# Performance work log

Hardware: AMD Instinct MI355X
Metric: run time of the kernel (lower is better)

## Reference

```python
import jax, jax.numpy as jnp
import numpy as np

# dims: B batches, N points/batch, S sampled points/batch, M image-projected points/batch,
# V voxels, (H,Wd) range-image size, HID hidden size, NSC scales, NCLS classes
B, N, S, M, V, H, Wd, HID, NSC, NCLS = 2, 120000, 40000, 30000, 100000, 256, 1024, 128, 4, 20


def setup_inputs() -> dict:
    key = jax.random.key(0)
    ks = jax.random.split(key, 24)
    f = jnp.float32
    w = lambda k, shp: (0.02 * jax.random.normal(k, shp, f))
    rows = jax.random.randint(ks[10], (B, M), 0, H, jnp.int32)
    cols = jax.random.randint(ks[11], (B, M), 0, Wd, jnp.int32)
    return {
        "pts_feat_layers": jax.random.normal(ks[0], (NSC, V, HID), f),
        "pts_sample_feat": jax.random.normal(ks[1], (NSC, B * S, HID), f),
        "img_latent_full": jax.random.normal(ks[2], (B, HID, H, Wd), f),
        "img_feat_layers": jax.random.normal(ks[3], (NSC, B * M, HID), f),
        "leaner_W": w(ks[4], (NSC, HID, HID)), "leaner_b": jnp.zeros((NSC, HID), f),
        "fcs1_W": w(ks[5], (NSC, 2 * HID, HID)), "fcs1_b": jnp.zeros((NSC, HID), f),
        "fcs2_W": w(ks[6], (NSC, HID, HID)), "fcs2_b": jnp.zeros((NSC, HID), f),
        "cls_W1": w(ks[7], (NSC * HID, 128)), "cls_b1": jnp.zeros((128,), f),
        "cls_W2": w(ks[8], (128, NCLS)), "cls_b2": jnp.zeros((NCLS,), f),
        "points_img": jnp.stack([rows, cols], axis=-1),              # [B,M,2]
        "point2img_index": jax.random.randint(ks[12], (B, M), 0, N, jnp.int32),
        "sample_index": jax.random.randint(ks[13], (B, S), 0, N, jnp.int32),
        "coors_inv": jax.random.randint(ks[14], (B * N,), 0, V, jnp.int32),
    }


def reference(pts_feat_layers, pts_sample_feat, img_latent_full, img_feat_layers,
              leaner_W, leaner_b, fcs1_W, fcs1_b, fcs2_W, fcs2_b,
              cls_W1, cls_b1, cls_W2, cls_b2,
              points_img, point2img_index, sample_index, coors_inv):
    dt = img_latent_full.dtype
    img_hw = jnp.transpose(img_latent_full, (0, 2, 3, 1))  # [B,H,Wd,HID]
    bar = jnp.arange(B)[:, None]
    # gather image features at projected pixel coords: [B,M,HID]
    img_at_pts = img_hw[bar, points_img[:, :, 0], points_img[:, :, 1]]
    # scatter image features to per-point slots (pts_img_batch_new): [B,N,HID]
    pimg = jax.vmap(lambda idx, v: jnp.zeros((N, HID), dt).at[idx].set(v))(point2img_index, img_at_pts)

    fuse_feats, enc_feats = [], []
    for i in range(NSC):
        # p2img_mapping_spsample: output values depend only on sampled feats + image gather
        sf = pts_sample_feat[i].reshape(B, S, HID)
        sp = jax.vmap(lambda idx, v: jnp.zeros((N, HID), dt).at[idx].set(v))(sample_index, sf)
        sp = sp + pimg  # sample_point_feat == sample_point_feat_f  [B,N,HID]
        # scatter fused point features back into voxel features, then gather per point
        pts_feat = pts_feat_layers[i].at[coors_inv].set(sp.reshape(B * N, HID))
        pts_point = pts_feat[coors_inv].reshape(B, N, HID)
        # p2img_mapping: gather the image-projected points per batch  [B*M,HID]
        pts_g = jnp.take_along_axis(pts_point, point2img_index[:, :, None], axis=1).reshape(B * M, HID)
        fl = jax.nn.relu(pts_g @ leaner_W[i] + leaner_b[i])
        fc = jnp.concatenate([img_feat_layers[i], fl], axis=1) @ fcs1_W[i] + fcs1_b[i]
        fw = jax.nn.sigmoid(fc @ fcs2_W[i] + fcs2_b[i])
        fuse_feats.append(jax.nn.relu(fc * fw))
        enc_feats.append(sp.reshape(B * N, HID))

    seg = jnp.concatenate(fuse_feats, axis=1)                       # [B*M, NSC*HID]
    img_seg_logits = jax.nn.relu(seg @ cls_W1 + cls_b1) @ cls_W2 + cls_b2  # [B*M, NCLS]
    output_3d = jnp.concatenate(enc_feats, axis=1)                  # [B*N, NSC*HID]
    return img_seg_logits, output_3d
```

## Files before the change

### kernel.cpp

```cpp
#include <hip/hip_runtime.h>
#include <hip/hip_bf16.h>
#include <math.h>

#define B_    2
#define N_    120000
#define S_    40000
#define M_    30000
#define V_    100000
#define H_    256
#define WD_   1024
#define HID_  128
#define NSC_  4
#define NCLS_ 20
#define BM_   60000
#define BS_   80000
#define BN_   240000

typedef __attribute__((ext_vector_type(8))) short bfrag8;
typedef __attribute__((ext_vector_type(4))) float facc4;
typedef __attribute__((ext_vector_type(4))) unsigned short usvec4;

__device__ __forceinline__ unsigned short f2bf(float f){
  unsigned u = __builtin_bit_cast(unsigned, f);
  u += 0x7fffu + ((u >> 16) & 1u);
  return (unsigned short)(u >> 16);
}
__device__ __forceinline__ float bf2f(unsigned short s){
  return __builtin_bit_cast(float, ((unsigned)s) << 16);
}

__global__ __launch_bounds__(256) void k_front(
    const float* __restrict__ img, const int* __restrict__ ptsimg,
    unsigned short* __restrict__ iap,
    const int* __restrict__ p2i, const int* __restrict__ si,
    const int* __restrict__ ci,
    int* __restrict__ win_p, int* __restrict__ win_s, int* __restrict__ win_c,
    const float* __restrict__ lW, const float* __restrict__ f1W,
    const float* __restrict__ f2W, const float* __restrict__ c1W,
    const float* __restrict__ c2W,
    unsigned short* __restrict__ lwT, unsigned short* __restrict__ f1T,
    unsigned short* __restrict__ f2T, unsigned short* __restrict__ c1T,
    unsigned short* __restrict__ c2T){
  int bid = blockIdx.x;
  if (bid < 938){
    int t = bid * 256 + threadIdx.x;
    if (t < BM_) atomicMax(&win_p[(t / M_) * N_ + p2i[t]], t);
    if (t < BS_) atomicMax(&win_s[(t / S_) * N_ + si[t]], t);
    if (t < BN_) atomicMax(&win_c[ci[t]], t);
    return;
  }
  if (bid < 2228){
    int t = (bid - 938) * 256 + threadIdx.x;
    if (t < 65536){
      int i = t >> 14, r = t & 16383, n = r >> 7, k = r & 127;
      lwT[i * 16384 + n * 128 + k] = f2bf(lW[i * 16384 + k * 128 + n]);
    } else if (t < 196608){
      int e = t - 65536;
      int i = e >> 15, r = e & 32767, n = r >> 8, k = r & 255;
      f1T[i * 32768 + n * 256 + k] = f2bf(f1W[i * 32768 + k * 128 + n]);
    } else if (t < 262144){
      int e = t - 196608;
      int i = e >> 14, r = e & 16383, n = r >> 7, k = r & 127;
      f2T[i * 16384 + n * 128 + k] = f2bf(f2W[i * 16384 + k * 128 + n]);
    } else if (t < 327680){
      int e = t - 262144;
      int n = e >> 9, k = e & 511;
      c1T[n * 512 + k] = f2bf(c1W[k * 128 + n]);
    } else if (t < 330240){
      int e = t - 327680;
      int n = e >> 7, k = e & 127;
      c2T[n * 128 + k] = f2bf(c2W[k * NCLS_ + n]);
    }
    return;
  }
  {
    int t = (bid - 2228) * 256 + threadIdx.x;
    int row = t >> 5, h4 = (t & 31) * 4;
    int b = row / M_;
    int r = ptsimg[row * 2 + 0];
    int c = ptsimg[row * 2 + 1];
    const float* base = img + (((size_t)b * HID_ + h4) * H_ + r) * WD_ + c;
    const size_t st = (size_t)H_ * WD_;
    float v0 = base[0], v1 = base[st], v2 = base[2 * st], v3 = base[3 * st];
    usvec4 o = {f2bf(v0), f2bf(v1), f2bf(v2), f2bf(v3)};
    *(usvec4*)(iap + (size_t)row * HID_ + h4) = o;
    return;
  }
}

__global__ __launch_bounds__(256) void k_o3d(const float* __restrict__ samp,
    const int* __restrict__ win_s, const int* __restrict__ win_p,
    const unsigned short* __restrict__ iap, float* __restrict__ o3d){
  int t = blockIdx.x * 256 + threadIdx.x;
  int j = t >> 5, q = t & 31;
  int sj = win_s[j], pj = win_p[j];
  facc4 iv = {0.f, 0.f, 0.f, 0.f};
  if (pj >= 0){
    usvec4 u = *(const usvec4*)(iap + (size_t)pj * HID_ + q * 4);
    iv.x = bf2f(u.x); iv.y = bf2f(u.y); iv.z = bf2f(u.z); iv.w = bf2f(u.w);
  }
  #pragma unroll
  for (int i = 0; i < NSC_; i++){
    facc4 v = iv;
    if (sj >= 0){
      facc4 s = *(const facc4*)(samp + ((size_t)i * BS_ + sj) * HID_ + q * 4);
      v += s;
    }
    __builtin_nontemporal_store(v, (facc4*)(o3d + (size_t)j * (NSC_ * HID_) + i * HID_ + q * 4));
  }
}

__global__ __launch_bounds__(256, 3) void k_scales(
    const float* __restrict__ samp, const unsigned short* __restrict__ iap,
    const int* __restrict__ win_p, const int* __restrict__ win_s,
    const int* __restrict__ win_c, const int* __restrict__ p2i,
    const int* __restrict__ ci, const float* __restrict__ imgf,
    const unsigned short* __restrict__ lwT, const float* __restrict__ lb,
    const unsigned short* __restrict__ f1T, const float* __restrict__ f1b,
    const unsigned short* __restrict__ f2T, const float* __restrict__ f2b,
    unsigned short* __restrict__ seg){
  __shared__ char lds[49152];
  char* actL = lds + 32768;
  const int i  = blockIdx.x & 3;
  const int rb = blockIdx.x >> 2;
  const int lane = threadIdx.x & 63, wv = threadIdx.x >> 6;
  const int rl = lane & 15, kg = lane >> 4;
  const int rowBase = rb * 64 + wv * 16;
  const int row = rowBase + rl;
  const bool rv = row < BM_;
  const int lr = wv * 16 + rl;

  {
    const char* src = (const char*)(lwT + (size_t)i * 16384);
    for (int c = threadIdx.x; c < 2048; c += 256){
      int byte = c << 4; int n = byte >> 8;
      *(bfrag8*)(lds + (byte ^ ((n & 7) << 4))) = *(const bfrag8*)(src + byte);
    }
  }
  bfrag8 afr[4];
  {
    int g = 0;
    if (rv){ int b = row >= M_; g = win_c[ci[b * N_ + p2i[row]]]; }
    int sj = rv ? win_s[g] : -1;
    int pj = rv ? win_p[g] : -1;
    const float* sp = samp + ((size_t)i * BS_ + (sj < 0 ? 0 : sj)) * HID_;
    const unsigned short* pp = iap + (size_t)(pj < 0 ? 0 : pj) * HID_;
    #pragma unroll
    for (int kc = 0; kc < 4; kc++){
      int k0 = kc * 32 + kg * 8;
      facc4 s0 = {0,0,0,0}, s1 = {0,0,0,0};
      if (sj >= 0){ s0 = *(const facc4*)(sp + k0); s1 = *(const facc4*)(sp + k0 + 4); }
      float g0=0,g1=0,g2=0,g3=0,g4=0,g5=0,g6=0,g7=0;
      if (pj >= 0){
        usvec4 u0 = *(const usvec4*)(pp + k0);
        usvec4 u1 = *(const usvec4*)(pp + k0 + 4);
        g0=bf2f(u0.x); g1=bf2f(u0.y); g2=bf2f(u0.z); g3=bf2f(u0.w);
        g4=bf2f(u1.x); g5=bf2f(u1.y); g6=bf2f(u1.z); g7=bf2f(u1.w);
      }
      bfrag8 a;
      a[0]=(short)f2bf(s0.x+g0); a[1]=(short)f2bf(s0.y+g1);
      a[2]=(short)f2bf(s0.z+g2); a[3]=(short)f2bf(s0.w+g3);
      a[4]=(short)f2bf(s1.x+g4); a[5]=(short)f2bf(s1.y+g5);
      a[6]=(short)f2bf(s1.z+g6); a[7]=(short)f2bf(s1.w+g7);
      afr[kc] = a;
    }
  }
  __syncthreads();
  facc4 accL[8];
  #pragma unroll
  for (int ct = 0; ct < 8; ct++) accL[ct] = (facc4){0.f,0.f,0.f,0.f};
  #pragma unroll
  for (int kc = 0; kc < 4; kc++){
    int k0 = kc * 32 + kg * 8;
    #pragma unroll
    for (int ct = 0; ct < 8; ct++){
      int col = ct * 16 + rl;
      int byte = (col << 8) + (k0 << 1);
      bfrag8 b = *(const bfrag8*)(lds + (byte ^ ((col & 7) << 4)));
      accL[ct] = __builtin_amdgcn_mfma_f32_16x16x32_bf16(afr[kc], b, accL[ct], 0, 0, 0);
    }
  }
  __syncthreads();
  {
    const float* bias = lb + i * HID_;
    #pragma unroll
    for (int ct = 0; ct < 8; ct++){
      int col = ct * 16 + rl;
      float bv = bias[col];
      #pragma unroll
      for (int r = 0; r < 4; r++){
        int ar = wv * 16 + kg * 4 + r;
        float v = accL[ct][r] + bv; v = v > 0.f ? v : 0.f;
        int byte = ar * 256 + col * 2;
        *(unsigned short*)(actL + (byte ^ ((ar & 7) << 4))) = f2bf(v);
      }
    }
    const char* src = (const char*)(f1T + (size_t)i * 32768);
    for (int c = threadIdx.x; c < 2048; c += 256){
      int n = c >> 4, off = (c & 15) << 4;
      *(bfrag8*)(lds + ((n * 256 + off) ^ ((n & 7) << 4))) =
          *(const bfrag8*)(src + (size_t)n * 512 + off);
    }
  }
  __syncthreads();
  facc4 accF[8];
  #pragma unroll
  for (int ct = 0; ct < 8; ct++) accF[ct] = (facc4){0.f,0.f,0.f,0.f};
  {
    const float* a1 = imgf + ((size_t)i * BM_ + (rv ? row : 0)) * HID_;
    #pragma unroll
    for (int kc = 0; kc < 4; kc++){
      int kk = kc * 32 + kg * 8;
      bfrag8 a = (bfrag8){0,0,0,0,0,0,0,0};
      if (rv){
        facc4 s0 = *(const facc4*)(a1 + kk);
        facc4 s1 = *(const facc4*)(a1 + kk + 4);
        a[0]=(short)f2bf(s0.x); a[1]=(short)f2bf(s0.y); a[2]=(short)f2bf(s0.z); a[3]=(short)f2bf(s0.w);
        a[4]=(short)f2bf(s1.x); a[5]=(short)f2bf(s1.y); a[6]=(short)f2bf(s1.z); a[7]=(short)f2bf(s1.w);
      }
      #pragma unroll
      for (int ct = 0; ct < 8; ct++){
        int col = ct * 16 + rl;
        int byte = (col << 8) + (kk << 1);
        bfrag8 b = *(const bfrag8*)(lds + (byte ^ ((col & 7) << 4)));
        accF[ct] = __builtin_amdgcn_mfma_f32_16x16x32_bf16(a, b, accF[ct], 0, 0, 0);
      }
    }
  }
  __syncthreads();
  {
    const char* src = (const char*)(f1T + (size_t)i * 32768) + 256;
    for (int c = threadIdx.x; c < 2048; c += 256){
      int n = c >> 4, off = (c & 15) << 4;
      *(bfrag8*)(lds + ((n * 256 + off) ^ ((n & 7) << 4))) =
          *(const bfrag8*)(src + (size_t)n * 512 + off);
    }
  }
  __syncthreads();
  #pragma unroll
  for (int kc = 0; kc < 4; kc++){
    int kl = kc * 32 + kg * 8;
    int byteA = lr * 256 + kl * 2;
    bfrag8 a = *(const bfrag8*)(actL + (byteA ^ ((lr & 7) << 4)));
    #pragma unroll
    for (int ct = 0; ct < 8; ct++){
      int col = ct * 16 + rl;
      int byte = (col << 8) + (kl << 1);
      bfrag8 b = *(const bfrag8*)(lds + (byte ^ ((col & 7) << 4)));
      accF[ct] = __builtin_amdgcn_mfma_f32_16x16x32_bf16(a, b, accF[ct], 0, 0, 0);
    }
  }
  __syncthreads();
  {
    const float* bias = f1b + i * HID_;
    #pragma unroll
    for (int ct = 0; ct < 8; ct++){
      int col = ct * 16 + rl;
      float bv = bias[col];
      #pragma unroll
      for (int r = 0; r < 4; r++){
        int ar = wv * 16 + kg * 4 + r;
        float v = accF[ct][r] + bv;
        accF[ct][r] = v;
        int byte = ar * 256 + col * 2;
        *(unsigned short*)(actL + (byte ^ ((ar & 7) << 4))) = f2bf(v);
      }
    }
    const char* src = (const char*)(f2T + (size_t)i * 16384);
    for (int c = threadIdx.x; c < 2048; c += 256){
      int byte = c << 4; int n = byte >> 8;
      *(bfrag8*)(lds + (byte ^ ((n & 7) << 4))) = *(const bfrag8*)(src + byte);
    }
  }
  __syncthreads();
  facc4 accT[8];
  #pragma unroll
  for (int ct = 0; ct < 8; ct++) accT[ct] = (facc4){0.f,0.f,0.f,0.f};
  #pragma unroll
  for (int kc = 0; kc < 4; kc++){
    int kk = kc * 32 + kg * 8;
    int byteA = lr * 256 + kk * 2;
    bfrag8 a = *(const bfrag8*)(actL + (byteA ^ ((lr & 7) << 4)));
    #pragma unroll
    for (int ct = 0; ct < 8; ct++){
      int col = ct * 16 + rl;
      int byte = (col << 8) + (kk << 1);
      bfrag8 b = *(const bfrag8*)(lds + (byte ^ ((col & 7) << 4)));
      accT[ct] = __builtin_amdgcn_mfma_f32_16x16x32_bf16(a, b, accT[ct], 0, 0, 0);
    }
  }
  {
    const float* bias2 = f2b + i * HID_;
    #pragma unroll
    for (int ct = 0; ct < 8; ct++){
      int col = ct * 16 + rl;
      float bv2 = bias2[col];
      #pragma unroll
      for (int r = 0; r < 4; r++){
        int orow = rowBase + kg * 4 + r;
        if (orow < BM_){
          float tv = accT[ct][r] + bv2;
          float fw = 1.f / (1.f + expf(-tv));
          float u = accF[ct][r] * fw;
          u = u > 0.f ? u : 0.f;
          seg[(size_t)orow * (NSC_ * HID_) + i * HID_ + col] = f2bf(u);
        }
      }
    }
  }
}

__global__ __launch_bounds__(256, 3) void k_cls(const unsigned short* __restrict__ seg,
    const unsigned short* __restrict__ c1T, const float* __restrict__ c1b,
    const unsigned short* __restrict__ c2T, const float* __restrict__ c2b,
    float* __restrict__ logits){
  __shared__ char lds[49152];
  char* actL = lds + 32768;
  const int lane = threadIdx.x & 63, wv = threadIdx.x >> 6;
  const int rl = lane & 15, kg = lane >> 4;
  const int rowBase = blockIdx.x * 64 + wv * 16;
  const int row = rowBase + rl;
  const bool rv = row < BM_;
  const unsigned short* ar = seg + (size_t)(rv ? row : 0) * 512;
  facc4 acc[8];
  #pragma unroll
  for (int ct = 0; ct < 8; ct++) acc[ct] = (facc4){0.f,0.f,0.f,0.f};
  for (int ph = 0; ph < 4; ph++){
    if (ph) __syncthreads();
    for (int c = threadIdx.x; c < 2048; c += 256){
      int n = c >> 4, off = (c & 15) << 4;
      *(bfrag8*)(lds + ((n * 256 + off) ^ ((n & 7) << 4))) =
          *(const bfrag8*)((const char*)c1T + (size_t)n * 1024 + ph * 256 + off);
    }
    __syncthreads();
    #pragma unroll
    for (int kc = 0; kc < 4; kc++){
      int kl = kc * 32 + kg * 8;
      bfrag8 a = (bfrag8){0,0,0,0,0,0,0,0};
      if (rv) a = *(const bfrag8*)(ar + ph * 128 + kl);
      #pragma unroll
      for (int ct = 0; ct < 8; ct++){
        int col = ct * 16 + rl;
        int byte = (col << 8) + (kl << 1);
        bfrag8 b = *(const bfrag8*)(lds + (byte ^ ((col & 7) << 4)));
        acc[ct] = __builtin_amdgcn_mfma_f32_16x16x32_bf16(a, b, acc[ct], 0, 0, 0);
      }
    }
  }
  __syncthreads();
  #pragma unroll
  for (int ct = 0; ct < 8; ct++){
    int col = ct * 16 + rl;
    float bv = c1b[col];
    #pragma unroll
    for (int r = 0; r < 4; r++){
      int arr = wv * 16 + kg * 4 + r;
      float v = acc[ct][r] + bv; v = v > 0.f ? v : 0.f;
      int byte = arr * 256 + col * 2;
      *(unsigned short*)(actL + (byte ^ ((arr & 7) << 4))) = f2bf(v);
    }
  }
  for (int c = threadIdx.x; c < 320; c += 256)
    *(bfrag8*)(lds + (c << 4)) = *(const bfrag8*)((const char*)c2T + (c << 4));
  __syncthreads();
  {
    int t = threadIdx.x;
    int lrd = t >> 2, n0 = (t & 3) * 5;
    int orow = blockIdx.x * 64 + lrd;
    if (orow < BM_){
      float accD[5];
      #pragma unroll
      for (int q = 0; q < 5; q++) accD[q] = c2b[n0 + q];
      #pragma unroll
      for (int k8 = 0; k8 < 16; k8++){
        int byteA = lrd * 256 + (k8 << 4);
        bfrag8 hv = *(const bfrag8*)(actL + (byteA ^ ((lrd & 7) << 4)));
        #pragma unroll
        for (int q = 0; q < 5; q++){
          bfrag8 w8 = *(const bfrag8*)(lds + (n0 + q) * 256 + (k8 << 4));
          #pragma unroll
          for (int e = 0; e < 8; e++)
            accD[q] += bf2f((unsigned short)hv[e]) * bf2f((unsigned short)w8[e]);
        }
      }
      #pragma unroll
      for (int q = 0; q < 5; q++)
        logits[(size_t)orow * NCLS_ + n0 + q] = accD[q];
    }
  }
}

extern "C" void kernel_launch(void* const* d_in, const int* in_sizes, int n_in,
                              void* d_out, int out_size, void* d_ws, size_t ws_size,
                              hipStream_t stream){
  const float* samp = (const float*)d_in[1];
  const float* img  = (const float*)d_in[2];
  const float* imgf = (const float*)d_in[3];
  const float* lW   = (const float*)d_in[4];
  const float* lb   = (const float*)d_in[5];
  const float* f1W  = (const float*)d_in[6];
  const float* f1b  = (const float*)d_in[7];
  const float* f2W  = (const float*)d_in[8];
  const float* f2b  = (const float*)d_in[9];
  const float* c1W  = (const float*)d_in[10];
  const float* c1b  = (const float*)d_in[11];
  const float* c2W  = (const float*)d_in[12];
  const float* c2b  = (const float*)d_in[13];
  const int* ptsimg = (const int*)d_in[14];
  const int* p2i    = (const int*)d_in[15];
  const int* si     = (const int*)d_in[16];
  const int* ci     = (const int*)d_in[17];

  char* ws = (char*)d_ws;
  int*   win_p = (int*)(ws + 0);
  int*   win_s = (int*)(ws + 960000);
  int*   win_c = (int*)(ws + 1920000);
  unsigned short* iap = (unsigned short*)(ws + 2320128);
  unsigned short* seg = (unsigned short*)(ws + 17680384);
  unsigned short* lwT = (unsigned short*)(ws + 79120512);
  unsigned short* f1T = lwT + 65536;
  unsigned short* f2T = f1T + 131072;
  unsigned short* c1T = f2T + 65536;
  unsigned short* c2T = c1T + 65536;

  float* logits = (float*)d_out;
  float* o3d    = (float*)d_out + (size_t)BM_ * NCLS_;

  (void)hipMemsetAsync(ws, 0xFF, 2320000, stream);
  k_front  <<<9728,  256, 0, stream>>>(img, ptsimg, iap, p2i, si, ci,
                                       win_p, win_s, win_c,
                                       lW, f1W, f2W, c1W, c2W,
                                       lwT, f1T, f2T, c1T, c2T);
  k_o3d    <<<30000, 256, 0, stream>>>(samp, win_s, win_p, iap, o3d);
  k_scales <<<3752,  256, 0, stream>>>(samp, iap, win_p, win_s, win_c, p2i, ci,
                                       imgf, lwT, lb, f1T, f1b, f2T, f2b, seg);
  k_cls    <<<938,   256, 0, stream>>>(seg, c1T, c1b, c2T, c2b, logits);
}
```

Baseline: 459.9 us.

## Fuse per-scale MLP and classifier into one kernel, batch o3d rows

Merges k_scales and k_cls into a single kernel. Each 64-row block loops over the four scales and accumulates the first classifier layer in registers, so the bf16 seg intermediate is no longer written to and re-read from global memory. Weights are staged into LDS in 64-column halves, which cuts LDS to 32KB and allows occupancy hint 5, at the cost of extra barriers and a serialized scale loop with fewer blocks. k_o3d now handles four output rows per thread, and the image gather in k_front handles both batches per thread, which reduces launch and index overhead.

```diff
diff --git a/kernel.cpp b/kernel.cpp
--- a/kernel.cpp
+++ b/kernel.cpp
@@ -27,6 +27,30 @@
 }
 __device__ __forceinline__ float bf2f(unsigned short s){
   return __builtin_bit_cast(float, ((unsigned)s) << 16);
+}
+
+__device__ __forceinline__ void stageW(char* wbuf, const char* src, int nstride, int tid){
+  #pragma unroll
+  for (int c0 = 0; c0 < 4; c0++){
+    int c = c0 * 256 + tid;
+    int nloc = c >> 4, off = (c & 15) << 4;
+    *(bfrag8*)(wbuf + (((nloc << 8) + off) ^ ((nloc & 7) << 4))) =
+        *(const bfrag8*)(src + (size_t)nloc * nstride + off);
+  }
+}
+
+__device__ __forceinline__ void mfmaHalf(facc4* acc4, const bfrag8* afr,
+                                         const char* wbuf, int rl, int kg){
+  #pragma unroll
+  for (int kc = 0; kc < 4; kc++){
+    int k2 = (kc * 32 + kg * 8) << 1;
+    #pragma unroll
+    for (int ctl = 0; ctl < 4; ctl++){
+      int nloc = ctl * 16 + rl;
+      bfrag8 b = *(const bfrag8*)(wbuf + (((nloc << 8) + k2) ^ ((nloc & 7) << 4)));
+      acc4[ctl] = __builtin_amdgcn_mfma_f32_16x16x32_bf16(afr[kc], b, acc4[ctl], 0, 0, 0);
+    }
+  }
 }
 
 __global__ __launch_bounds__(256) void k_front(
@@ -75,15 +99,18 @@
   }
   {
     int t = (bid - 2228) * 256 + threadIdx.x;
-    int row = t >> 5, h4 = (t & 31) * 4;
-    int b = row / M_;
-    int r = ptsimg[row * 2 + 0];
-    int c = ptsimg[row * 2 + 1];
-    const float* base = img + (((size_t)b * HID_ + h4) * H_ + r) * WD_ + c;
+    int r0 = t >> 5, h4 = (t & 31) * 4;
     const size_t st = (size_t)H_ * WD_;
-    float v0 = base[0], v1 = base[st], v2 = base[2 * st], v3 = base[3 * st];
-    usvec4 o = {f2bf(v0), f2bf(v1), f2bf(v2), f2bf(v3)};
-    *(usvec4*)(iap + (size_t)row * HID_ + h4) = o;
+    #pragma unroll
+    for (int half = 0; half < 2; half++){
+      int row = r0 + half * 30000;
+      int r = ptsimg[row * 2 + 0];
+      int c = ptsimg[row * 2 + 1];
+      const float* base = img + (((size_t)half * HID_ + h4) * H_ + r) * WD_ + c;
+      float v0 = base[0], v1 = base[st], v2 = base[2 * st], v3 = base[3 * st];
+      usvec4 o = {f2bf(v0), f2bf(v1), f2bf(v2), f2bf(v3)};
+      *(usvec4*)(iap + (size_t)row * HID_ + h4) = o;
+    }
     return;
   }
 }
@@ -92,25 +119,35 @@
     const int* __restrict__ win_s, const int* __restrict__ win_p,
     const unsigned short* __restrict__ iap, float* __restrict__ o3d){
   int t = blockIdx.x * 256 + threadIdx.x;
-  int j = t >> 5, q = t & 31;
-  int sj = win_s[j], pj = win_p[j];
-  facc4 iv = {0.f, 0.f, 0.f, 0.f};
-  if (pj >= 0){
-    usvec4 u = *(const usvec4*)(iap + (size_t)pj * HID_ + q * 4);
-    iv.x = bf2f(u.x); iv.y = bf2f(u.y); iv.z = bf2f(u.z); iv.w = bf2f(u.w);
+  int jg = t >> 5, q = t & 31;
+  int j0 = jg << 2;
+  int sjv[4], pjv[4];
+  #pragma unroll
+  for (int jj = 0; jj < 4; jj++){ sjv[jj] = win_s[j0 + jj]; pjv[jj] = win_p[j0 + jj]; }
+  facc4 iv[4];
+  #pragma unroll
+  for (int jj = 0; jj < 4; jj++){
+    facc4 v = {0.f, 0.f, 0.f, 0.f};
+    if (pjv[jj] >= 0){
+      usvec4 u = *(const usvec4*)(iap + (size_t)pjv[jj] * HID_ + q * 4);
+      v.x = bf2f(u.x); v.y = bf2f(u.y); v.z = bf2f(u.z); v.w = bf2f(u.w);
+    }
+    iv[jj] = v;
   }
   #pragma unroll
   for (int i = 0; i < NSC_; i++){
-    facc4 v = iv;
-    if (sj >= 0){
-      facc4 s = *(const facc4*)(samp + ((size_t)i * BS_ + sj) * HID_ + q * 4);
-      v += s;
-    }
-    __builtin_nontemporal_store(v, (facc4*)(o3d + (size_t)j * (NSC_ * HID_) + i * HID_ + q * 4));
-  }
-}
-
-__global__ __launch_bounds__(256, 3) void k_scales(
+    #pragma unroll
+    for (int jj = 0; jj < 4; jj++){
+      facc4 v = iv[jj];
+      if (sjv[jj] >= 0)
+        v += *(const facc4*)(samp + ((size_t)i * BS_ + sjv[jj]) * HID_ + q * 4);
+      __builtin_nontemporal_store(v,
+          (facc4*)(o3d + (size_t)(j0 + jj) * (NSC_ * HID_) + i * HID_ + q * 4));
+    }
+  }
+}
+
+__global__ __launch_bounds__(256, 5) void k_fused(
     const float* __restrict__ samp, const unsigned short* __restrict__ iap,
     const int* __restrict__ win_p, const int* __restrict__ win_s,
     const int* __restrict__ win_c, const int* __restrict__ p2i,
@@ -118,254 +155,210 @@
     const unsigned short* __restrict__ lwT, const float* __restrict__ lb,
     const unsigned short* __restrict__ f1T, const float* __restrict__ f1b,
     const unsigned short* __restrict__ f2T, const float* __restrict__ f2b,
-    unsigned short* __restrict__ seg){
-  __shared__ char lds[49152];
-  char* actL = lds + 32768;
-  const int i  = blockIdx.x & 3;
-  const int rb = blockIdx.x >> 2;
-  const int lane = threadIdx.x & 63, wv = threadIdx.x >> 6;
-  const int rl = lane & 15, kg = lane >> 4;
-  const int rowBase = rb * 64 + wv * 16;
-  const int row = rowBase + rl;
-  const bool rv = row < BM_;
-  const int lr = wv * 16 + rl;
-
-  {
-    const char* src = (const char*)(lwT + (size_t)i * 16384);
-    for (int c = threadIdx.x; c < 2048; c += 256){
-      int byte = c << 4; int n = byte >> 8;
-      *(bfrag8*)(lds + (byte ^ ((n & 7) << 4))) = *(const bfrag8*)(src + byte);
-    }
-  }
-  bfrag8 afr[4];
-  {
-    int g = 0;
-    if (rv){ int b = row >= M_; g = win_c[ci[b * N_ + p2i[row]]]; }
-    int sj = rv ? win_s[g] : -1;
-    int pj = rv ? win_p[g] : -1;
-    const float* sp = samp + ((size_t)i * BS_ + (sj < 0 ? 0 : sj)) * HID_;
-    const unsigned short* pp = iap + (size_t)(pj < 0 ? 0 : pj) * HID_;
-    #pragma unroll
-    for (int kc = 0; kc < 4; kc++){
-      int k0 = kc * 32 + kg * 8;
-      facc4 s0 = {0,0,0,0}, s1 = {0,0,0,0};
-      if (sj >= 0){ s0 = *(const facc4*)(sp + k0); s1 = *(const facc4*)(sp + k0 + 4); }
-      float g0=0,g1=0,g2=0,g3=0,g4=0,g5=0,g6=0,g7=0;
-      if (pj >= 0){
-        usvec4 u0 = *(const usvec4*)(pp + k0);
-        usvec4 u1 = *(const usvec4*)(pp + k0 + 4);
-        g0=bf2f(u0.x); g1=bf2f(u0.y); g2=bf2f(u0.z); g3=bf2f(u0.w);
-        g4=bf2f(u1.x); g5=bf2f(u1.y); g6=bf2f(u1.z); g7=bf2f(u1.w);
-      }
-      bfrag8 a;
-      a[0]=(short)f2bf(s0.x+g0); a[1]=(short)f2bf(s0.y+g1);
-      a[2]=(short)f2bf(s0.z+g2); a[3]=(short)f2bf(s0.w+g3);
-      a[4]=(short)f2bf(s1.x+g4); a[5]=(short)f2bf(s1.y+g5);
-      a[6]=(short)f2bf(s1.z+g6); a[7]=(short)f2bf(s1.w+g7);
-      afr[kc] = a;
-    }
-  }
-  __syncthreads();
-  facc4 accL[8];
-  #pragma unroll
-  for (int ct = 0; ct < 8; ct++) accL[ct] = (facc4){0.f,0.f,0.f,0.f};
-  #pragma unroll
-  for (int kc = 0; kc < 4; kc++){
-    int k0 = kc * 32 + kg * 8;
-    #pragma unroll
-    for (int ct = 0; ct < 8; ct++){
-      int col = ct * 16 + rl;
-      int byte = (col << 8) + (k0 << 1);
-      bfrag8 b = *(const bfrag8*)(lds + (byte ^ ((col & 7) << 4)));
-      accL[ct] = __builtin_amdgcn_mfma_f32_16x16x32_bf16(afr[kc], b, accL[ct], 0, 0, 0);
-    }
-  }
-  __syncthreads();
-  {
-    const float* bias = lb + i * HID_;
-    #pragma unroll
-    for (int ct = 0; ct < 8; ct++){
-      int col = ct * 16 + rl;
-      float bv = bias[col];
-      #pragma unroll
-      for (int r = 0; r < 4; r++){
-        int ar = wv * 16 + kg * 4 + r;
-        float v = accL[ct][r] + bv; v = v > 0.f ? v : 0.f;
-        int byte = ar * 256 + col * 2;
-        *(unsigned short*)(actL + (byte ^ ((ar & 7) << 4))) = f2bf(v);
-      }
-    }
-    const char* src = (const char*)(f1T + (size_t)i * 32768);
-    for (int c = threadIdx.x; c < 2048; c += 256){
-      int n = c >> 4, off = (c & 15) << 4;
-      *(bfrag8*)(lds + ((n * 256 + off) ^ ((n & 7) << 4))) =
-          *(const bfrag8*)(src + (size_t)n * 512 + off);
-    }
-  }
-  __syncthreads();
-  facc4 accF[8];
-  #pragma unroll
-  for (int ct = 0; ct < 8; ct++) accF[ct] = (facc4){0.f,0.f,0.f,0.f};
-  {
-    const float* a1 = imgf + ((size_t)i * BM_ + (rv ? row : 0)) * HID_;
-    #pragma unroll
-    for (int kc = 0; kc < 4; kc++){
-      int kk = kc * 32 + kg * 8;
-      bfrag8 a = (bfrag8){0,0,0,0,0,0,0,0};
-      if (rv){
-        facc4 s0 = *(const facc4*)(a1 + kk);
-        facc4 s1 = *(const facc4*)(a1 + kk + 4);
-        a[0]=(short)f2bf(s0.x); a[1]=(short)f2bf(s0.y); a[2]=(short)f2bf(s0.z); a[3]=(short)f2bf(s0.w);
-        a[4]=(short)f2bf(s1.x); a[5]=(short)f2bf(s1.y); a[6]=(short)f2bf(s1.z); a[7]=(short)f2bf(s1.w);
-      }
-      #pragma unroll
-      for (int ct = 0; ct < 8; ct++){
-        int col = ct * 16 + rl;
-        int byte = (col << 8) + (kk << 1);
-        bfrag8 b = *(const bfrag8*)(lds + (byte ^ ((col & 7) << 4)));
-        accF[ct] = __builtin_amdgcn_mfma_f32_16x16x32_bf16(a, b, accF[ct], 0, 0, 0);
-      }
-    }
-  }
-  __syncthreads();
-  {
-    const char* src = (const char*)(f1T + (size_t)i * 32768) + 256;
-    for (int c = threadIdx.x; c < 2048; c += 256){
-      int n = c >> 4, off = (c & 15) << 4;
-      *(bfrag8*)(lds + ((n * 256 + off) ^ ((n & 7) << 4))) =
-          *(const bfrag8*)(src + (size_t)n * 512 + off);
-    }
-  }
-  __syncthreads();
-  #pragma unroll
-  for (int kc = 0; kc < 4; kc++){
-    int kl = kc * 32 + kg * 8;
-    int byteA = lr * 256 + kl * 2;
-    bfrag8 a = *(const bfrag8*)(actL + (byteA ^ ((lr & 7) << 4)));
-    #pragma unroll
-    for (int ct = 0; ct < 8; ct++){
-      int col = ct * 16 + rl;
-      int byte = (col << 8) + (kl << 1);
-      bfrag8 b = *(const bfrag8*)(lds + (byte ^ ((col & 7) << 4)));
-      accF[ct] = __builtin_amdgcn_mfma_f32_16x16x32_bf16(a, b, accF[ct], 0, 0, 0);
-    }
-  }
-  __syncthreads();
-  {
-    const float* bias = f1b + i * HID_;
-    #pragma unroll
-    for (int ct = 0; ct < 8; ct++){
-      int col = ct * 16 + rl;
-      float bv = bias[col];
-      #pragma unroll
-      for (int r = 0; r < 4; r++){
-        int ar = wv * 16 + kg * 4 + r;
-        float v = accF[ct][r] + bv;
-        accF[ct][r] = v;
-        int byte = ar * 256 + col * 2;
-        *(unsigned short*)(actL + (byte ^ ((ar & 7) << 4))) = f2bf(v);
-      }
-    }
-    const char* src = (const char*)(f2T + (size_t)i * 16384);
-    for (int c = threadIdx.x; c < 2048; c += 256){
-      int byte = c << 4; int n = byte >> 8;
-      *(bfrag8*)(lds + (byte ^ ((n & 7) << 4))) = *(const bfrag8*)(src + byte);
-    }
-  }
-  __syncthreads();
-  facc4 accT[8];
-  #pragma unroll
-  for (int ct = 0; ct < 8; ct++) accT[ct] = (facc4){0.f,0.f,0.f,0.f};
-  #pragma unroll
-  for (int kc = 0; kc < 4; kc++){
-    int kk = kc * 32 + kg * 8;
-    int byteA = lr * 256 + kk * 2;
-    bfrag8 a = *(const bfrag8*)(actL + (byteA ^ ((lr & 7) << 4)));
-    #pragma unroll
-    for (int ct = 0; ct < 8; ct++){
-      int col = ct * 16 + rl;
-      int byte = (col << 8) + (kk << 1);
-      bfrag8 b = *(const bfrag8*)(lds + (byte ^ ((col & 7) << 4)));
-      accT[ct] = __builtin_amdgcn_mfma_f32_16x16x32_bf16(a, b, accT[ct], 0, 0, 0);
-    }
-  }
-  {
-    const float* bias2 = f2b + i * HID_;
-    #pragma unroll
-    for (int ct = 0; ct < 8; ct++){
-      int col = ct * 16 + rl;
-      float bv2 = bias2[col];
-      #pragma unroll
-      for (int r = 0; r < 4; r++){
-        int orow = rowBase + kg * 4 + r;
-        if (orow < BM_){
-          float tv = accT[ct][r] + bv2;
-          float fw = 1.f / (1.f + expf(-tv));
-          float u = accF[ct][r] * fw;
-          u = u > 0.f ? u : 0.f;
-          seg[(size_t)orow * (NSC_ * HID_) + i * HID_ + col] = f2bf(u);
-        }
-      }
-    }
-  }
-}
-
-__global__ __launch_bounds__(256, 3) void k_cls(const unsigned short* __restrict__ seg,
     const unsigned short* __restrict__ c1T, const float* __restrict__ c1b,
     const unsigned short* __restrict__ c2T, const float* __restrict__ c2b,
     float* __restrict__ logits){
-  __shared__ char lds[49152];
-  char* actL = lds + 32768;
-  const int lane = threadIdx.x & 63, wv = threadIdx.x >> 6;
+  __shared__ char lds[32768];
+  char* wbuf = lds;
+  char* actL = lds + 16384;
+  const int tid = threadIdx.x;
+  const int lane = tid & 63, wv = tid >> 6;
   const int rl = lane & 15, kg = lane >> 4;
   const int rowBase = blockIdx.x * 64 + wv * 16;
   const int row = rowBase + rl;
   const bool rv = row < BM_;
-  const unsigned short* ar = seg + (size_t)(rv ? row : 0) * 512;
-  facc4 acc[8];
-  #pragma unroll
-  for (int ct = 0; ct < 8; ct++) acc[ct] = (facc4){0.f,0.f,0.f,0.f};
-  for (int ph = 0; ph < 4; ph++){
-    if (ph) __syncthreads();
-    for (int c = threadIdx.x; c < 2048; c += 256){
-      int n = c >> 4, off = (c & 15) << 4;
-      *(bfrag8*)(lds + ((n * 256 + off) ^ ((n & 7) << 4))) =
-          *(const bfrag8*)((const char*)c1T + (size_t)n * 1024 + ph * 256 + off);
+  const int lr = wv * 16 + rl;
+
+  int sj = -1, pj = -1;
+  if (rv){
+    int b = row >= M_;
+    int g = win_c[ci[b * N_ + p2i[row]]];
+    sj = win_s[g]; pj = win_p[g];
+  }
+  usvec4 ppv[8];
+  #pragma unroll
+  for (int e = 0; e < 8; e++) ppv[e] = (usvec4){0, 0, 0, 0};
+  if (pj >= 0){
+    const unsigned short* pp = iap + (size_t)pj * HID_;
+    #pragma unroll
+    for (int kc = 0; kc < 4; kc++){
+      int k0 = kc * 32 + kg * 8;
+      ppv[2 * kc]     = *(const usvec4*)(pp + k0);
+      ppv[2 * kc + 1] = *(const usvec4*)(pp + k0 + 4);
+    }
+  }
+
+  facc4 accC[8];
+  #pragma unroll
+  for (int a = 0; a < 8; a++) accC[a] = (facc4){0.f, 0.f, 0.f, 0.f};
+
+  #pragma unroll 1
+  for (int i = 0; i < NSC_; i++){
+    bfrag8 afrL[4];
+    {
+      const float* sp = samp + ((size_t)i * BS_ + (sj < 0 ? 0 : sj)) * HID_;
+      #pragma unroll
+      for (int kc = 0; kc < 4; kc++){
+        int k0 = kc * 32 + kg * 8;
+        facc4 s0 = {0,0,0,0}, s1 = {0,0,0,0};
+        if (sj >= 0){ s0 = *(const facc4*)(sp + k0); s1 = *(const facc4*)(sp + k0 + 4); }
+        usvec4 u0 = ppv[2 * kc], u1 = ppv[2 * kc + 1];
+        bfrag8 a;
+        a[0] = (short)f2bf(s0.x + bf2f(u0.x)); a[1] = (short)f2bf(s0.y + bf2f(u0.y));
+        a[2] = (short)f2bf(s0.z + bf2f(u0.z)); a[3] = (short)f2bf(s0.w + bf2f(u0.w));
+        a[4] = (short)f2bf(s1.x + bf2f(u1.x)); a[5] = (short)f2bf(s1.y + bf2f(u1.y));
+        a[6] = (short)f2bf(s1.z + bf2f(u1.z)); a[7] = (short)f2bf(s1.w + bf2f(u1.w));
+        afrL[kc] = a;
+      }
+    }
+    bfrag8 afrI[4];
+    {
+      const float* a1 = imgf + ((size_t)i * BM_ + (rv ? row : 0)) * HID_;
+      #pragma unroll
+      for (int kc = 0; kc < 4; kc++){
+        int k0 = kc * 32 + kg * 8;
+        facc4 s0 = {0,0,0,0}, s1 = {0,0,0,0};
+        if (rv){ s0 = *(const facc4*)(a1 + k0); s1 = *(const facc4*)(a1 + k0 + 4); }
+        bfrag8 a;
+        a[0]=(short)f2bf(s0.x); a[1]=(short)f2bf(s0.y); a[2]=(short)f2bf(s0.z); a[3]=(short)f2bf(s0.w);
+        a[4]=(short)f2bf(s1.x); a[5]=(short)f2bf(s1.y); a[6]=(short)f2bf(s1.z); a[7]=(short)f2bf(s1.w);
+        afrI[kc] = a;
+      }
+    }
+
+    facc4 accL[8];
+    #pragma unroll
+    for (int a = 0; a < 8; a++) accL[a] = (facc4){0.f, 0.f, 0.f, 0.f};
+    #pragma unroll
+    for (int h = 0; h < 2; h++){
+      stageW(wbuf, (const char*)(lwT + (size_t)i * 16384) + (size_t)h * 64 * 256, 256, tid);
+      __syncthreads();
+      mfmaHalf(&accL[h * 4], afrL, wbuf, rl, kg);
+      __syncthreads();
+    }
+    {
+      const float* bias = lb + i * HID_;
+      #pragma unroll
+      for (int a = 0; a < 8; a++){
+        int col = (a >> 2) * 64 + (a & 3) * 16 + rl;
+        float bv = bias[col];
+        #pragma unroll
+        for (int r = 0; r < 4; r++){
+          int ar = wv * 16 + kg * 4 + r;
+          float v = accL[a][r] + bv; v = v > 0.f ? v : 0.f;
+          int byte = ar * 256 + col * 2;
+          *(unsigned short*)(actL + (byte ^ ((ar & 7) << 4))) = f2bf(v);
+        }
+      }
+    }
+    facc4 accF[8];
+    #pragma unroll
+    for (int a = 0; a < 8; a++) accF[a] = (facc4){0.f, 0.f, 0.f, 0.f};
+    #pragma unroll
+    for (int h = 0; h < 2; h++){
+      stageW(wbuf, (const char*)(f1T + (size_t)i * 32768) + (size_t)h * 64 * 512, 512, tid);
+      __syncthreads();
+      mfmaHalf(&accF[h * 4], afrI, wbuf, rl, kg);
+      __syncthreads();
+    }
+    bfrag8 afrF[4];
+    #pragma unroll
+    for (int kc = 0; kc < 4; kc++){
+      int byteA = lr * 256 + ((kc * 32 + kg * 8) << 1);
+      afrF[kc] = *(const bfrag8*)(actL + (byteA ^ ((lr & 7) << 4)));
+    }
+    #pragma unroll
+    for (int h = 0; h < 2; h++){
+      stageW(wbuf, (const char*)(f1T + (size_t)i * 32768) + (size_t)h * 64 * 512 + 256, 512, tid);
+      __syncthreads();
+      mfmaHalf(&accF[h * 4], afrF, wbuf, rl, kg);
+      __syncthreads();
+    }
+    {
+      const float* bias = f1b + i * HID_;
+      #pragma unroll
+      for (int a = 0; a < 8; a++){
+        int col = (a >> 2) * 64 + (a & 3) * 16 + rl;
+        float bv = bias[col];
+        #pragma unroll
+        for (int r = 0; r < 4; r++){
+          int ar = wv * 16 + kg * 4 + r;
+          float v = accF[a][r] + bv;
+          accF[a][r] = v;
+          int byte = ar * 256 + col * 2;
+          *(unsigned short*)(actL + (byte ^ ((ar & 7) << 4))) = f2bf(v);
+        }
+      }
+    }
+    facc4 accT[8];
+    #pragma unroll
+    for (int a = 0; a < 8; a++) accT[a] = (facc4){0.f, 0.f, 0.f, 0.f};
+    bfrag8 afrC[4];
+    #pragma unroll
+    for (int h = 0; h < 2; h++){
+      stageW(wbuf, (const char*)(f2T + (size_t)i * 16384) + (size_t)h * 64 * 256, 256, tid);
+      __syncthreads();
+      if (h == 0){
+        #pragma unroll
+        for (int kc = 0; kc < 4; kc++){
+          int byteA = lr * 256 + ((kc * 32 + kg * 8) << 1);
+          afrC[kc] = *(const bfrag8*)(actL + (byteA ^ ((lr & 7) << 4)));
+        }
+      }
+      mfmaHalf(&accT[h * 4], afrC, wbuf, rl, kg);
+      __syncthreads();
+    }
+    {
+      const float* bias2 = f2b + i * HID_;
+      #pragma unroll
+      for (int a = 0; a < 8; a++){
+        int col = (a >> 2) * 64 + (a & 3) * 16 + rl;
+        float bv2 = bias2[col];
+        #pragma unroll
+        for (int r = 0; r < 4; r++){
+          int ar = wv * 16 + kg * 4 + r;
+          float tv = accT[a][r] + bv2;
+          float fw = 1.f / (1.f + expf(-tv));
+          float u = accF[a][r] * fw;
+          u = u > 0.f ? u : 0.f;
+          int byte = ar * 256 + col * 2;
+          *(unsigned short*)(actL + (byte ^ ((ar & 7) << 4))) = f2bf(u);
+        }
+      }
     }
     __syncthreads();
+    bfrag8 afrU[4];
     #pragma unroll
     for (int kc = 0; kc < 4; kc++){
-      int kl = kc * 32 + kg * 8;
-      bfrag8 a = (bfrag8){0,0,0,0,0,0,0,0};
-      if (rv) a = *(const bfrag8*)(ar + ph * 128 + kl);
-      #pragma unroll
-      for (int ct = 0; ct < 8; ct++){
-        int col = ct * 16 + rl;
-        int byte = (col << 8) + (kl << 1);
-        bfrag8 b = *(const bfrag8*)(lds + (byte ^ ((col & 7) << 4)));
-        acc[ct] = __builtin_amdgcn_mfma_f32_16x16x32_bf16(a, b, acc[ct], 0, 0, 0);
-      }
-    }
-  }
-  __syncthreads();
-  #pragma unroll
-  for (int ct = 0; ct < 8; ct++){
-    int col = ct * 16 + rl;
+      int byteA = lr * 256 + ((kc * 32 + kg * 8) << 1);
+      afrU[kc] = *(const bfrag8*)(actL + (byteA ^ ((lr & 7) << 4)));
+    }
+    #pragma unroll
+    for (int h = 0; h < 2; h++){
+      stageW(wbuf, (const char*)c1T + (size_t)h * 64 * 1024 + i * 256, 1024, tid);
+      __syncthreads();
+      mfmaHalf(&accC[h * 4], afrU, wbuf, rl, kg);
+      __syncthreads();
+    }
+  }
+
+  #pragma unroll
+  for (int a = 0; a < 8; a++){
+    int col = (a >> 2) * 64 + (a & 3) * 16 + rl;
     float bv = c1b[col];
     #pragma unroll
     for (int r = 0; r < 4; r++){
-      int arr = wv * 16 + kg * 4 + r;
-      float v = acc[ct][r] + bv; v = v > 0.f ? v : 0.f;
-      int byte = arr * 256 + col * 2;
-      *(unsigned short*)(actL + (byte ^ ((arr & 7) << 4))) = f2bf(v);
-    }
-  }
-  for (int c = threadIdx.x; c < 320; c += 256)
-    *(bfrag8*)(lds + (c << 4)) = *(const bfrag8*)((const char*)c2T + (c << 4));
+      int ar = wv * 16 + kg * 4 + r;
+      float v = accC[a][r] + bv; v = v > 0.f ? v : 0.f;
+      int byte = ar * 256 + col * 2;
+      *(unsigned short*)(actL + (byte ^ ((ar & 7) << 4))) = f2bf(v);
+    }
+  }
+  for (int c = tid; c < 320; c += 256)
+    *(bfrag8*)(wbuf + (c << 4)) = *(const bfrag8*)((const char*)c2T + (c << 4));
   __syncthreads();
   {
-    int t = threadIdx.x;
-    int lrd = t >> 2, n0 = (t & 3) * 5;
+    int lrd = tid >> 2, n0 = (tid & 3) * 5;
     int orow = blockIdx.x * 64 + lrd;
     if (orow < BM_){
       float accD[5];
@@ -377,7 +370,7 @@
         bfrag8 hv = *(const bfrag8*)(actL + (byteA ^ ((lrd & 7) << 4)));
         #pragma unroll
         for (int q = 0; q < 5; q++){
-          bfrag8 w8 = *(const bfrag8*)(lds + (n0 + q) * 256 + (k8 << 4));
+          bfrag8 w8 = *(const bfrag8*)(wbuf + (n0 + q) * 256 + (k8 << 4));
           #pragma unroll
           for (int e = 0; e < 8; e++)
             accD[q] += bf2f((unsigned short)hv[e]) * bf2f((unsigned short)w8[e]);
@@ -416,8 +409,7 @@
   int*   win_s = (int*)(ws + 960000);
   int*   win_c = (int*)(ws + 1920000);
   unsigned short* iap = (unsigned short*)(ws + 2320128);
-  unsigned short* seg = (unsigned short*)(ws + 17680384);
-  unsigned short* lwT = (unsigned short*)(ws + 79120512);
+  unsigned short* lwT = (unsigned short*)(ws + 17680384);
   unsigned short* f1T = lwT + 65536;
   unsigned short* f2T = f1T + 131072;
   unsigned short* c1T = f2T + 65536;
@@ -427,12 +419,12 @@
   float* o3d    = (float*)d_out + (size_t)BM_ * NCLS_;
 
   (void)hipMemsetAsync(ws, 0xFF, 2320000, stream);
-  k_front  <<<9728,  256, 0, stream>>>(img, ptsimg, iap, p2i, si, ci,
-                                       win_p, win_s, win_c,
-                                       lW, f1W, f2W, c1W, c2W,
-                                       lwT, f1T, f2T, c1T, c2T);
-  k_o3d    <<<30000, 256, 0, stream>>>(samp, win_s, win_p, iap, o3d);
-  k_scales <<<3752,  256, 0, stream>>>(samp, iap, win_p, win_s, win_c, p2i, ci,
-                                       imgf, lwT, lb, f1T, f1b, f2T, f2b, seg);
-  k_cls    <<<938,   256, 0, stream>>>(seg, c1T, c1b, c2T, c2b, logits);
-}
+  k_front<<<5978, 256, 0, stream>>>(img, ptsimg, iap, p2i, si, ci,
+                                    win_p, win_s, win_c,
+                                    lW, f1W, f2W, c1W, c2W,
+                                    lwT, f1T, f2T, c1T, c2T);
+  k_o3d  <<<7500, 256, 0, stream>>>(samp, win_s, win_p, iap, o3d);
+  k_fused<<<938,  256, 0, stream>>>(samp, iap, win_p, win_s, win_c, p2i, ci,
+                                    imgf, lwT, lb, f1T, f1b, f2T, f2b,
+                                    c1T, c1b, c2T, c2b, logits);
+}
```

Result: slower. 780.6 us (+69.7%).
